# Performance work log

Hardware: AMD Instinct MI355X
Metric: run time of the kernel (lower is better)

The kernel has to match this reference:

```python
import jax, jax.numpy as jnp
import numpy as np

BIAS = 0.1  # init kwarg `bias`
B = 8192


def setup_inputs() -> dict:
    key = jax.random.key(0)
    k1, k2, k3 = jax.random.split(key, 3)
    predictions = jax.random.normal(k1, (B,), dtype=jnp.float32)
    correct_output = jax.random.normal(k2, (B,), dtype=jnp.float32)
    weight = jax.random.uniform(k3, (B,), dtype=jnp.float32)
    return {"predictions": predictions, "correct_output": correct_output, "weight": weight}


def reference(predictions, correct_output, weight):
    # pairwise diffs: [B, B], diff[m, n] = pred_m - pred_n
    diff = predictions[:, None] - predictions[None, :]
    gt_diff = correct_output[:, None] - correct_output[None, :]
    # r = +1 if pred_m > pred_n, -1 if pred_m < pred_n, else -sign(gt_m - gt_n)
    r = jnp.where(diff > 0, 1.0, jnp.where(diff < 0, -1.0, -jnp.sign(gt_diff)))
    # weighted by average pair weight
    r = r * (weight[:, None] + weight[None, :]) * 0.5
    loss = jnp.maximum(0.0, BIAS - r * diff)  # hinge per pair
    return jnp.sum(loss) / (B * B)
```

## Files before the change

kernel.cpp:

```cpp
#include <hip/hip_runtime.h>


#define BIAS_F 0.1f

constexpr int TPB = 256;
constexpr int NPT = 8;
constexpr int TN  = TPB * NPT;
constexpr int TM  = 32;

__global__ __launch_bounds__(TPB) void pair_loss_kernel(
    const float* __restrict__ pred,
    const float* __restrict__ weight,
    float* __restrict__ partial,
    int B)
{
    const int n_base = blockIdx.x * TN;
    const int m_base = blockIdx.y * TM;
    const int t = threadIdx.x;

    float pn[NPT], wnh[NPT], mask[NPT];
    #pragma unroll
    for (int j = 0; j < NPT; ++j) {
        int n = n_base + j * TPB + t;
        bool ok = (n < B);
        int nc = ok ? n : 0;
        pn[j]   = pred[nc];
        wnh[j]  = weight[nc] * 0.5f;
        mask[j] = ok ? 1.0f : 0.0f;
    }

    float acc[NPT];
    #pragma unroll
    for (int j = 0; j < NPT; ++j) acc[j] = 0.0f;

    const int m_end = (m_base + TM <= B) ? TM : (B - m_base);
    #pragma unroll 4
    for (int i = 0; i < m_end; ++i) {
        const int m = m_base + i;
        const float pm  = pred[m];
        const float wmh = weight[m] * 0.5f;
        #pragma unroll
        for (int j = 0; j < NPT; ++j) {
            float d  = pm - pn[j];
            float w  = wmh + wnh[j];
            float th = fmaf(-w, fabsf(d), BIAS_F);
            acc[j] += fmaxf(th, 0.0f);
        }
    }

    float s = 0.0f;
    #pragma unroll
    for (int j = 0; j < NPT; ++j) s += mask[j] * acc[j];

    #pragma unroll
    for (int off = 32; off > 0; off >>= 1)
        s += __shfl_down(s, off, 64);

    __shared__ float lds[TPB / 64];
    const int lane = t & 63, wid = t >> 6;
    if (lane == 0) lds[wid] = s;
    __syncthreads();
    if (t == 0) {
        float bs = 0.0f;
        #pragma unroll
        for (int w = 0; w < TPB / 64; ++w) bs += lds[w];
        partial[blockIdx.y * gridDim.x + blockIdx.x] = bs;
    }
}

__global__ __launch_bounds__(256) void reduce_kernel(
    const float* __restrict__ partial, int n, float* __restrict__ out, int B)
{
    double s = 0.0;
    for (int i = threadIdx.x; i < n; i += 256) s += (double)partial[i];
    #pragma unroll
    for (int off = 32; off > 0; off >>= 1)
        s += __shfl_down(s, off, 64);
    __shared__ double lds[4];
    const int lane = threadIdx.x & 63, wid = threadIdx.x >> 6;
    if (lane == 0) lds[wid] = s;
    __syncthreads();
    if (threadIdx.x == 0) {
        double tot = lds[0] + lds[1] + lds[2] + lds[3];
        double inv = 1.0 / ((double)B * (double)B);
        out[0] = (float)(tot * inv);
    }
}

extern "C" void kernel_launch(void* const* d_in, const int* in_sizes, int n_in,
                              void* d_out, int out_size, void* d_ws, size_t ws_size,
                              hipStream_t stream) {
    const float* pred   = (const float*)d_in[0];
    const float* weight = (const float*)d_in[2];
    float* out = (float*)d_out;
    const int B = in_sizes[0];

    const int tilesN = (B + TN - 1) / TN;
    const int tilesM = (B + TM - 1) / TM;
    float* partial = (float*)d_ws;

    dim3 grid(tilesN, tilesM);
    pair_loss_kernel<<<grid, TPB, 0, stream>>>(pred, weight, partial, B);
    reduce_kernel<<<1, 256, 0, stream>>>(partial, tilesN * tilesM, out, B);
}
```

Measured before the change: 16.94 us.

## Exploit pair symmetry to compute only upper-triangle tiles

Uses the symmetry of the pairwise hinge loss to evaluate only pairs with n > m. Tiles entirely below the diagonal write zero and exit early, and the final reduce doubles the sum and adds the diagonal term B*BIAS. NPT drops from 8 to 2 to give a finer grid so the triangle is covered with less waste. Diagonal and boundary tiles take a masked slow path, and the grid now has four times as many blocks and partials to reduce.

```diff
diff --git a/kernel.cpp b/kernel.cpp
--- a/kernel.cpp
+++ b/kernel.cpp
@@ -4,7 +4,7 @@
 #define BIAS_F 0.1f
 
 constexpr int TPB = 256;
-constexpr int NPT = 8;
+constexpr int NPT = 2;
 constexpr int TN  = TPB * NPT;
 constexpr int TM  = 32;
 
@@ -14,43 +14,68 @@
     float* __restrict__ partial,
     int B)
 {
-    const int n_base = blockIdx.x * TN;
-    const int m_base = blockIdx.y * TM;
+    const int n0 = blockIdx.x * TN;
+    const int m0 = blockIdx.y * TM;
+    const int bid = blockIdx.y * gridDim.x + blockIdx.x;
     const int t = threadIdx.x;
 
-    float pn[NPT], wnh[NPT], mask[NPT];
+    if (n0 + TN - 1 <= m0) {
+        if (t == 0) partial[bid] = 0.0f;
+        return;
+    }
+
+    float pn[NPT], wnh[NPT];
+    int nidx[NPT];
     #pragma unroll
     for (int j = 0; j < NPT; ++j) {
-        int n = n_base + j * TPB + t;
+        int n = n0 + j * TPB + t;
         bool ok = (n < B);
         int nc = ok ? n : 0;
         pn[j]   = pred[nc];
         wnh[j]  = weight[nc] * 0.5f;
-        mask[j] = ok ? 1.0f : 0.0f;
+        nidx[j] = ok ? n : -1;
     }
 
     float acc[NPT];
     #pragma unroll
     for (int j = 0; j < NPT; ++j) acc[j] = 0.0f;
 
-    const int m_end = (m_base + TM <= B) ? TM : (B - m_base);
-    #pragma unroll 4
-    for (int i = 0; i < m_end; ++i) {
-        const int m = m_base + i;
-        const float pm  = pred[m];
-        const float wmh = weight[m] * 0.5f;
-        #pragma unroll
-        for (int j = 0; j < NPT; ++j) {
-            float d  = pm - pn[j];
-            float w  = wmh + wnh[j];
-            float th = fmaf(-w, fabsf(d), BIAS_F);
-            acc[j] += fmaxf(th, 0.0f);
+    const bool clean = (n0 >= m0 + TM) && (n0 + TN <= B) && (m0 + TM <= B);
+
+    if (clean) {
+        #pragma unroll 4
+        for (int i = 0; i < TM; ++i) {
+            const int m = m0 + i;
+            const float pm  = pred[m];
+            const float wmh = weight[m] * 0.5f;
+            #pragma unroll
+            for (int j = 0; j < NPT; ++j) {
+                float d  = pm - pn[j];
+                float w  = wmh + wnh[j];
+                float th = fmaf(-w, fabsf(d), BIAS_F);
+                acc[j] += fmaxf(th, 0.0f);
+            }
+        }
+    } else {
+        const int m_end = (m0 + TM <= B) ? TM : (B - m0);
+        for (int i = 0; i < m_end; ++i) {
+            const int m = m0 + i;
+            const float pm  = pred[m];
+            const float wmh = weight[m] * 0.5f;
+            #pragma unroll
+            for (int j = 0; j < NPT; ++j) {
+                float d  = pm - pn[j];
+                float w  = wmh + wnh[j];
+                float th = fmaf(-w, fabsf(d), BIAS_F);
+                float h  = fmaxf(th, 0.0f);
+                acc[j] += (nidx[j] > m) ? h : 0.0f;
+            }
         }
     }
 
-    float s = 0.0f;
+    float s = acc[0];
     #pragma unroll
-    for (int j = 0; j < NPT; ++j) s += mask[j] * acc[j];
+    for (int j = 1; j < NPT; ++j) s += acc[j];
 
     #pragma unroll
     for (int off = 32; off > 0; off >>= 1)
@@ -64,7 +89,7 @@
         float bs = 0.0f;
         #pragma unroll
         for (int w = 0; w < TPB / 64; ++w) bs += lds[w];
-        partial[blockIdx.y * gridDim.x + blockIdx.x] = bs;
+        partial[bid] = bs;
     }
 }
 
@@ -82,8 +107,8 @@
     __syncthreads();
     if (threadIdx.x == 0) {
         double tot = lds[0] + lds[1] + lds[2] + lds[3];
-        double inv = 1.0 / ((double)B * (double)B);
-        out[0] = (float)(tot * inv);
+        double full = 2.0 * tot + (double)B * (double)BIAS_F;
+        out[0] = (float)(full / ((double)B * (double)B));
     }
 }
 
```

Measured after the change: 21.30 us. 1.26x slower.
